# Optimization experiments

Hardware: AMD Instinct MI355X
Metric: run time of the kernel (lower is better)

## Reference

```python
import jax, jax.numpy as jnp
import numpy as np

B, S = 16, 768
DCOG, DENV, NENV = 64, 32, 8
D, N, L, FF, NC = 512, 64, 6, 2048, 1
DIL = (1, 2, 4, 8)
EPS = 1e-5


def _layer_norm(x, g, b):
    m = x.mean(-1, keepdims=True)
    v = ((x - m) ** 2).mean(-1, keepdims=True)
    return (x - m) * jax.lax.rsqrt(v + EPS) * g + b


def _conv1d(x, w, b, d):
    # x: (B, D, S), w: (O, I, K); 'same' padding = (K-1)*d//2 = d for K=3
    y = jax.lax.conv_general_dilated(x, w, (1,), [(d, d)], rhs_dilation=(d,),
                                     dimension_numbers=('NCH', 'OIH', 'NCH'))
    return y + b[None, :, None]


def _combine(c1, c2):
    a1, b1 = c1
    a2, b2 = c2
    return a1 * a2, a2 * b1 + b2


def _forward(x_cog, cw1, cb1, cw2, cb2, env_emb, ew1, eb1, ew2, eb2,
             fw1, fb1, fw2, fb2, pos_enc, conv_w, conv_b, wm_w, wm_b,
             ssm_w, ssm_b, A_log, ffw1, ffb1, ffw2, ffb2,
             g1, be1, g2, be2, pw1, pb1, pw2, pb2, x_env):
    # Dual-channel feature processor (dropout = identity at eval)
    z = x_cog / jnp.maximum(jnp.linalg.norm(x_cog, axis=-1, keepdims=True), 1e-12)
    z = jnp.maximum(z @ cw1 + cb1, 0.0) @ cw2 + cb2
    e = env_emb[x_env].mean(-2)                      # (B,S,NENV,D) -> (B,S,D)
    e = jnp.maximum(e @ ew1 + eb1, 0.0) @ ew2 + eb2
    hf = jnp.concatenate([z, e], -1)
    hf = jnp.maximum(hf @ fw1 + fb1, 0.0) @ fw2 + fb2
    h = hf + pos_enc[:S][None]

    def layer_step(h, p):
        cw, cb, wmw, wmb, sw, sb, alog, w1, b1, w2, b2, g1_, be1_, g2_, be2_ = p
        # Multi-scale dilated conv
        xt = h.transpose(0, 2, 1)                    # (B, D, S)
        outs = [_conv1d(xt, cw[i], cb[i], DIL[i]) for i in range(4)]
        alpha = jax.nn.softmax(xt.mean(-1) @ wmw + wmb, -1)   # (B, 4)
        hm = sum(alpha[:, i, None, None] * outs[i] for i in range(4)).transpose(0, 2, 1)
        h1 = _layer_norm(hm + h, g1_, be1_)
        # Selective state-space (diagonal A), parallel associative scan
        proj = jnp.einsum('bsd,kdn->kbsn', h1, sw) + sb[:, None, None, :]
        delta, Bt, Ct = jax.nn.softplus(proj[0]), proj[1], proj[2]
        a = jnp.exp(alog[None, None, :] * delta)     # (B, S, N)
        bu = Bt * h1[..., :N]
        _, hs = jax.lax.associative_scan(_combine, (a, bu), axis=1)
        y = jnp.sum(Ct * hs, -1, keepdims=True)      # (B, S, 1)
        h2 = _layer_norm(y + h1, g2_, be2_)          # broadcast over D, as in torch
        return jnp.maximum(h2 @ w1 + b1, 0.0) @ w2 + b2 + h2, None

    h, _ = jax.lax.scan(layer_step, h, (conv_w, conv_b, wm_w, wm_b, ssm_w, ssm_b,
                                        A_log, ffw1, ffb1, ffw2, ffb2, g1, be1, g2, be2))
    hg = h.mean(1)                                   # adaptive avg pool over S
    return jnp.maximum(hg @ pw1 + pb1, 0.0) @ pw2 + pb2


def setup_inputs():
    ks = iter(jax.random.split(jax.random.key(0), 48))
    def rn(shape, s=0.02):
        return jax.random.normal(next(ks), shape, jnp.float32) * s
    return {
        'x_cog': rn((B, S, DCOG), 1.0),
        'cw1': rn((DCOG, D)), 'cb1': jnp.zeros(D), 'cw2': rn((D, D)), 'cb2': jnp.zeros(D),
        'env_emb': rn((DENV, D), 1.0),
        'ew1': rn((D, D)), 'eb1': jnp.zeros(D), 'ew2': rn((D, D)), 'eb2': jnp.zeros(D),
        'fw1': rn((2 * D, D)), 'fb1': jnp.zeros(D), 'fw2': rn((D, D)), 'fb2': jnp.zeros(D),
        'pos_enc': rn((1000, D), 1.0),
        'conv_w': rn((L, 4, D, D, 3)), 'conv_b': jnp.zeros((L, 4, D)),
        'wm_w': rn((L, D, 4)), 'wm_b': jnp.zeros((L, 4)),
        'ssm_w': rn((L, 3, D, N)), 'ssm_b': jnp.zeros((L, 3, N)),
        'A_log': -jnp.abs(rn((L, N), 1.0)),
        'ffw1': rn((L, D, FF)), 'ffb1': jnp.zeros((L, FF)),
        'ffw2': rn((L, FF, D)), 'ffb2': jnp.zeros((L, D)),
        'g1': jnp.ones((L, D)), 'be1': jnp.zeros((L, D)),
        'g2': jnp.ones((L, D)), 'be2': jnp.zeros((L, D)),
        'pw1': rn((D, D // 2)), 'pb1': jnp.zeros(D // 2),
        'pw2': rn((D // 2, NC)), 'pb2': jnp.zeros(NC),
        'x_env': jax.random.randint(next(ks), (B, S, NENV), 0, DENV, jnp.int32),
    }


def reference(x_cog, cw1, cb1, cw2, cb2, env_emb, ew1, eb1, ew2, eb2,
              fw1, fb1, fw2, fb2, pos_enc, conv_w, conv_b, wm_w, wm_b,
              ssm_w, ssm_b, A_log, ffw1, ffb1, ffw2, ffb2,
              g1, be1, g2, be2, pw1, pb1, pw2, pb2, x_env):
    return _forward(x_cog, cw1, cb1, cw2, cb2, env_emb, ew1, eb1, ew2, eb2,
                    fw1, fb1, fw2, fb2, pos_enc, conv_w, conv_b, wm_w, wm_b,
                    ssm_w, ssm_b, A_log, ffw1, ffb1, ffw2, ffb2,
                    g1, be1, g2, be2, pw1, pb1, pw2, pb2, x_env)
```

## Files before the change

### kernel.cpp

```cpp
#include <hip/hip_runtime.h>
#include <cstdint>
#include <cstddef>

namespace {

constexpr int B = 16, S = 768, BS = B * S, D = 512, FF = 2048, L = 6;
constexpr float EPS = 1e-5f;

typedef float f32x4 __attribute__((ext_vector_type(4)));
typedef _Float16 f16x8 __attribute__((ext_vector_type(8)));

__device__ __forceinline__ float wave_sum(float v) {
#pragma unroll
  for (int o = 32; o > 0; o >>= 1) v += __shfl_xor(v, o, 64);
  return v;
}

__device__ __forceinline__ short f16b(float x) {
  const _Float16 h = (_Float16)x;
  return __builtin_bit_cast(short, h);
}
__device__ __forceinline__ float h2f(short s) {
  return (float)__builtin_bit_cast(_Float16, s);
}

__device__ __forceinline__ void gload16(const void* g, void* l) {
  __builtin_amdgcn_global_load_lds(
      (const __attribute__((address_space(1))) void*)g,
      (__attribute__((address_space(3))) void*)l, 16, 0, 0);
}


template <bool RELU, bool PACK>
__global__ __launch_bounds__(256, 3) void gemm_h(
    const short* __restrict__ A, int lda, const short* __restrict__ Wt,
    int ldw, int Klen, const float* __restrict__ bias,
    short* __restrict__ ph, int ldp) {
  __shared__ alignas(16) short sAh[8192], sBh[8192];
  const int tid = threadIdx.x;
  const unsigned Nt = gridDim.x;
  const unsigned lin = blockIdx.y * Nt + blockIdx.x;
  const unsigned cpx = (Nt * gridDim.y) >> 3;
  const unsigned swz = (lin & 7) * cpx + (lin >> 3);
  const int bn = (int)(swz % Nt) * 128, bm = (int)(swz / Nt) * 128;
  const int wave = tid >> 6, lane = tid & 63;
  const int wr = (wave >> 1) * 64, wc = (wave & 1) * 64;
  const int lr = lane & 15, sl = lane >> 4;
  const short* Ab = A + (size_t)bm * lda;
  const short* Wb = Wt + (size_t)bn * ldw;
  f32x4 acc[4][4] = {};
  for (int kk = 0; kk < Klen; kk += 64) {
#pragma unroll
    for (int jj = 0; jj < 4; ++jj) {
      const int G = jj * 256 + tid;
      const int srow = G >> 3, sl0 = G & 7;
      const int gsl = sl0 ^ (srow & 7);
      const int dst = G * 8;
      gload16(Ab + (size_t)srow * lda + kk + gsl * 8, &sAh[dst]);
      gload16(Wb + (size_t)srow * ldw + kk + gsl * 8, &sBh[dst]);
    }
    __syncthreads();
#pragma unroll
    for (int ks = 0; ks < 2; ++ks) {
      f16x8 aH[4], bH[4];
#pragma unroll
      for (int m = 0; m < 4; ++m) {
        const int r = wr + m * 16 + lr;
        aH[m] = *(const f16x8*)&sAh[r * 64 + (((ks * 4 + sl) ^ (r & 7)) * 8)];
      }
#pragma unroll
      for (int n = 0; n < 4; ++n) {
        const int r = wc + n * 16 + lr;
        bH[n] = *(const f16x8*)&sBh[r * 64 + (((ks * 4 + sl) ^ (r & 7)) * 8)];
      }
#pragma unroll
      for (int m = 0; m < 4; ++m)
#pragma unroll
        for (int n = 0; n < 4; ++n)
          acc[m][n] = __builtin_amdgcn_mfma_f32_16x16x32_f16(aH[m], bH[n],
                                                             acc[m][n], 0, 0, 0);
    }
    __syncthreads();
  }
  const int r4 = sl * 4;
#pragma unroll
  for (int m = 0; m < 4; ++m) {
#pragma unroll
    for (int r = 0; r < 4; ++r) {
      const int mm = bm + wr + m * 16 + r4 + r;
#pragma unroll
      for (int n = 0; n < 4; ++n) {
        const int col = bn + wc + n * 16 + lr;
        float v = acc[m][n][r] + bias[col];
        if (RELU) v = fmaxf(v, 0.f);
        if (PACK) ph[(size_t)mm * ldp + col] = f16b(v);
      }
    }
  }
}

template <bool RELU, int RESM, bool PACK, bool CSUM, int BK>
__global__ __launch_bounds__(256, 3) void gemm_h64(
    const short* __restrict__ A, int lda, const short* __restrict__ Wt,
    int ldw, int Klen, const float* __restrict__ bias,
    const float* __restrict__ resid, const short* __restrict__ residS,
    int ldr, int rmod, short* __restrict__ ph, int ldp,
    float* __restrict__ part) {
  constexpr int GPR = BK / 8;
  constexpr int AR = 128 * GPR / 256;
  constexpr int BR = 64 * GPR / 256;
  constexpr int KS = BK / 32;
  __shared__ alignas(16) short sAh[128 * BK], sBh[64 * BK];
  __shared__ float csLds[2][64];
  const int tid = threadIdx.x;
  const unsigned Nt = gridDim.x;
  const unsigned lin = blockIdx.y * Nt + blockIdx.x;
  const unsigned cpx = (Nt * gridDim.y) >> 3;
  const unsigned swz = (lin & 7) * cpx + (lin >> 3);
  const int bn = (int)(swz % Nt) * 64, bmt = (int)(swz / Nt);
  const int bm = bmt * 128;
  const int wave = tid >> 6, lane = tid & 63;
  const int wr = (wave >> 1) * 64, wc = (wave & 1) * 32;
  const int lr = lane & 15, sl = lane >> 4;
  const short* Ab = A + (size_t)bm * lda;
  const short* Wb = Wt + (size_t)bn * ldw;
  f32x4 acc[4][2] = {};
  for (int kk = 0; kk < Klen; kk += BK) {
#pragma unroll
    for (int jj = 0; jj < AR; ++jj) {
      const int G = jj * 256 + tid;
      const int srow = G / GPR, sl0 = G % GPR;
      const int gsl = sl0 ^ (srow & (GPR - 1));
      gload16(Ab + (size_t)srow * lda + kk + gsl * 8, &sAh[G * 8]);
    }
#pragma unroll
    for (int jj = 0; jj < BR; ++jj) {
      const int G = jj * 256 + tid;
      const int srow = G / GPR, sl0 = G % GPR;
      const int gsl = sl0 ^ (srow & (GPR - 1));
      gload16(Wb + (size_t)srow * ldw + kk + gsl * 8, &sBh[G * 8]);
    }
    __syncthreads();
#pragma unroll
    for (int ks = 0; ks < KS; ++ks) {
      f16x8 aH[4], bH[2];
#pragma unroll
      for (int m = 0; m < 4; ++m) {
        const int r = wr + m * 16 + lr;
        aH[m] = *(const f16x8*)
            &sAh[r * BK + (((ks * 4 + sl) ^ (r & (GPR - 1))) * 8)];
      }
#pragma unroll
      for (int n = 0; n < 2; ++n) {
        const int r = wc + n * 16 + lr;
        bH[n] = *(const f16x8*)
            &sBh[r * BK + (((ks * 4 + sl) ^ (r & (GPR - 1))) * 8)];
      }
#pragma unroll
      for (int m = 0; m < 4; ++m)
#pragma unroll
        for (int n = 0; n < 2; ++n)
          acc[m][n] = __builtin_amdgcn_mfma_f32_16x16x32_f16(aH[m], bH[n],
                                                             acc[m][n], 0, 0, 0);
    }
    __syncthreads();
  }
  const int r4 = sl * 4;
  float cs[2] = {0.f, 0.f};
#pragma unroll
  for (int m = 0; m < 4; ++m) {
#pragma unroll
    for (int r = 0; r < 4; ++r) {
      const int mm = bm + wr + m * 16 + r4 + r;
#pragma unroll
      for (int n = 0; n < 2; ++n) {
        const int col = bn + wc + n * 16 + lr;
        float v = acc[m][n][r] + bias[col];
        if (RELU) v = fmaxf(v, 0.f);
        if (RESM == 1) {
          const int rr = rmod ? (mm % rmod) : mm;
          v += resid[(size_t)rr * ldr + col];
        }
        if (RESM == 2) v += h2f(residS[(size_t)mm * ldr + col]);
        if (PACK) ph[(size_t)mm * ldp + col] = f16b(v);
        if (CSUM) cs[n] += v;
      }
    }
  }
  if constexpr (CSUM) {
#pragma unroll
    for (int n = 0; n < 2; ++n) {
      cs[n] += __shfl_xor(cs[n], 16, 64);
      cs[n] += __shfl_xor(cs[n], 32, 64);
    }
    if (sl == 0) {
      csLds[wave >> 1][wc + lr] = cs[0];
      csLds[wave >> 1][wc + 16 + lr] = cs[1];
    }
    __syncthreads();
    if (tid < 64)
      part[(size_t)bmt * 512 + bn + tid] = csLds[0][tid] + csLds[1][tid];
  }
}

__global__ __launch_bounds__(256, 3) void conv_zp_k(
    const short* __restrict__ hp, const short* __restrict__ wt8,
    const short* __restrict__ wmix, const float* __restrict__ alpha,
    const short* __restrict__ zpadS, short* __restrict__ P) {
  __shared__ alignas(16) short sAh[16384], sBh[8192];
  const int tid = threadIdx.x;
  const unsigned lin = blockIdx.x;
  const unsigned swz = (lin & 7) * 96 + (lin >> 3);
  const int bn = (int)(swz & 7) * 64;
  const int bmt = (int)(swz >> 3);
  const int b = bmt / 6, s0 = (bmt % 6) * 128, gm0 = bmt * 128;
  const int wave = tid >> 6, lane = tid & 63;
  const int wr = (wave >> 1) * 64, wc = (wave & 1) * 32;
  const int lr = lane & 15, sl = lane >> 4;
  const short* hb = hp + (size_t)b * S * 512;
  f32x4 accF[4][2] = {};
#pragma unroll
  for (int z = 0; z < 4; ++z) {
    const int dd = 1 << z;
    f32x4 acc[4][2] = {};
    for (int kk = 0; kk < 1024; kk += 128) {
      const int tap = kk >> 9;
      const int koff = kk & 511;
      const int off = tap ? dd : -dd;
#pragma unroll
      for (int jj = 0; jj < 8; ++jj) {
        const int G = jj * 256 + tid;
        const int srow = G >> 4, sl0 = G & 15;
        const int gsl = sl0 ^ (srow & 15);
        const int gs = s0 + srow + off;
        const bool inb = ((unsigned)gs < (unsigned)S);
        const short* aBase = hb + (size_t)gs * 512 + koff + gsl * 8;
        gload16(inb ? aBase : zpadS, &sAh[G * 8]);
      }
#pragma unroll
      for (int jj = 0; jj < 4; ++jj) {
        const int G = jj * 256 + tid;
        const int srow = G >> 4, sl0 = G & 15;
        const int gsl = sl0 ^ (srow & 15);
        gload16(wt8 + ((size_t)((z * 2 + tap) * 512 + bn + srow)) * 512 +
                    koff + gsl * 8,
                &sBh[G * 8]);
      }
      __syncthreads();
#pragma unroll
      for (int ks = 0; ks < 4; ++ks) {
        f16x8 aH[4], bH[2];
#pragma unroll
        for (int m = 0; m < 4; ++m) {
          const int r = wr + m * 16 + lr;
          aH[m] = *(const f16x8*)
              &sAh[r * 128 + (((ks * 4 + sl) ^ (r & 15)) * 8)];
        }
#pragma unroll
        for (int n = 0; n < 2; ++n) {
          const int r = wc + n * 16 + lr;
          bH[n] = *(const f16x8*)
              &sBh[r * 128 + (((ks * 4 + sl) ^ (r & 15)) * 8)];
        }
#pragma unroll
        for (int m = 0; m < 4; ++m)
#pragma unroll
          for (int n = 0; n < 2; ++n)
            acc[m][n] = __builtin_amdgcn_mfma_f32_16x16x32_f16(
                aH[m], bH[n], acc[m][n], 0, 0, 0);
      }
      __syncthreads();
    }
    const float al = alpha[b * 4 + z];
#pragma unroll
    for (int m = 0; m < 4; ++m)
#pragma unroll
      for (int n = 0; n < 2; ++n)
#pragma unroll
        for (int r = 0; r < 4; ++r) accF[m][n][r] += al * acc[m][n][r];
  }
  const short* Wm = wmix + (size_t)b * 512 * 512;
  for (int kc = 0; kc < 512; kc += 128) {
#pragma unroll
    for (int jj = 0; jj < 8; ++jj) {
      const int G = jj * 256 + tid;
      const int srow = G >> 4, sl0 = G & 15;
      const int gsl = sl0 ^ (srow & 15);
      gload16(hb + (size_t)(s0 + srow) * 512 + kc + gsl * 8, &sAh[G * 8]);
    }
#pragma unroll
    for (int jj = 0; jj < 4; ++jj) {
      const int G = jj * 256 + tid;
      const int srow = G >> 4, sl0 = G & 15;
      const int gsl = sl0 ^ (srow & 15);
      gload16(Wm + (size_t)(bn + srow) * 512 + kc + gsl * 8, &sBh[G * 8]);
    }
    __syncthreads();
#pragma unroll
    for (int ks = 0; ks < 4; ++ks) {
      f16x8 aH[4], bH[2];
#pragma unroll
      for (int m = 0; m < 4; ++m) {
        const int r = wr + m * 16 + lr;
        aH[m] =
            *(const f16x8*)&sAh[r * 128 + (((ks * 4 + sl) ^ (r & 15)) * 8)];
      }
#pragma unroll
      for (int n = 0; n < 2; ++n) {
        const int r = wc + n * 16 + lr;
        bH[n] =
            *(const f16x8*)&sBh[r * 128 + (((ks * 4 + sl) ^ (r & 15)) * 8)];
      }
#pragma unroll
      for (int m = 0; m < 4; ++m)
#pragma unroll
        for (int n = 0; n < 2; ++n)
          accF[m][n] = __builtin_amdgcn_mfma_f32_16x16x32_f16(
              aH[m], bH[n], accF[m][n], 0, 0, 0);
    }
    __syncthreads();
  }
  const int r4 = sl * 4;
#pragma unroll
  for (int m = 0; m < 4; ++m)
#pragma unroll
    for (int r = 0; r < 4; ++r) {
      const int mm = gm0 + wr + m * 16 + r4 + r;
#pragma unroll
      for (int n = 0; n < 2; ++n)
        P[(size_t)mm * D + bn + wc + n * 16 + lr] = f16b(accF[m][n][r]);
    }
}

__global__ __launch_bounds__(256) void ln3_k(
    const short* __restrict__ P0, const short* __restrict__ hpk,
    const float* __restrict__ cbmix, const float* __restrict__ g1,
    const float* __restrict__ b1, const float* __restrict__ g2,
    const float* __restrict__ b2, short* __restrict__ pout) {
  const int row = blockIdx.x * 4 + (threadIdx.x >> 6);
  const int lane = threadIdx.x & 63;
  const int bb = row / S;
  const size_t base = (size_t)row * D;
  float v[8];
  float s = 0.f;
#pragma unroll
  for (int j = 0; j < 8; ++j) {
    const int c = lane + 64 * j;
    v[j] = h2f(P0[base + c]) + h2f(hpk[base + c]) + cbmix[(size_t)bb * D + c];
    s += v[j];
  }
  s = wave_sum(s);
  const float m1 = s * (1.f / D);
  float q = 0.f;
#pragma unroll
  for (int j = 0; j < 8; ++j) { const float d = v[j] - m1; q += d * d; }
  q = wave_sum(q);
  const float r1 = rsqrtf(q * (1.f / D) + EPS);
  float y[8];
  float s2 = 0.f;
#pragma unroll
  for (int j = 0; j < 8; ++j) {
    const int c = lane + 64 * j;
    y[j] = (v[j] - m1) * r1 * g1[c] + b1[c];
    s2 += y[j];
  }
  s2 = wave_sum(s2);
  const float m2 = s2 * (1.f / D);
  float q2 = 0.f;
#pragma unroll
  for (int j = 0; j < 8; ++j) { const float d = y[j] - m2; q2 += d * d; }
  q2 = wave_sum(q2);
  const float r2 = rsqrtf(q2 * (1.f / D) + EPS);
  short* prow = pout + base;
#pragma unroll
  for (int j = 0; j < 8; ++j) {
    const int c = lane + 64 * j;
    prow[c] = f16b((y[j] - m2) * r2 * g2[c] + b2[c]);
  }
}

__device__ __forceinline__ void pack_tile(const float* __restrict__ W,
                                          short* __restrict__ out, int K,
                                          int N, int n0, int k0) {
  __shared__ short t[64][68];
  const int ln = threadIdx.x & 63, w4 = threadIdx.x >> 6;
#pragma unroll
  for (int it = 0; it < 16; ++it) {
    const int kr = it * 4 + w4;
    t[kr][ln] = f16b(W[(size_t)(k0 + kr) * N + n0 + ln]);
  }
  __syncthreads();
#pragma unroll
  for (int it = 0; it < 16; ++it) {
    const int nr = it * 4 + w4;
    out[(size_t)(n0 + nr) * K + k0 + ln] = t[ln][nr];
  }
}

__global__ __launch_bounds__(256) void pack_wt_k(const float* __restrict__ W,
                                                 short* __restrict__ out,
                                                 int K, int N) {
  pack_tile(W, out, K, N, blockIdx.x * 64, blockIdx.y * 64);
}

__global__ __launch_bounds__(256) void pack_ff_all_k(
    const float* __restrict__ ffw1, const float* __restrict__ ffw2,
    short* __restrict__ outAll) {
  const int bid = blockIdx.x;
  const int l = bid >> 9;
  const int r = bid & 511;
  if (r < 256) {
    pack_tile(ffw1 + (size_t)l * D * FF, outAll + (size_t)l * 2097152, 512,
              2048, (r & 31) * 64, (r >> 5) * 64);
  } else {
    const int r2 = r - 256;
    pack_tile(ffw2 + (size_t)l * FF * D,
              outAll + (size_t)l * 2097152 + 1048576, 2048, 512,
              (r2 & 7) * 64, (r2 >> 3) * 64);
  }
}

__global__ __launch_bounds__(256) void pack_conv8_all_k(
    const float* __restrict__ cw, short* __restrict__ out) {
  const size_t idx = (size_t)blockIdx.x * 256 + threadIdx.x;
  const int c = (int)(idx & 511);
  const int o = (int)((idx >> 9) & 511);
  const int seg = (int)((idx >> 18) & 7);
  const int l = (int)(idx >> 21);
  const int z = seg >> 1, t = (seg & 1) * 2;
  out[idx] = f16b(cw[((size_t)l * 4 * D * D + ((size_t)z * D + o) * D + c) * 3 + t]);
}

__global__ __launch_bounds__(256) void wmix_k(const float* __restrict__ cw,
                                              const float* __restrict__ alpha,
                                              short* __restrict__ wm) {
  __shared__ float sal[64];
  if (threadIdx.x < 64) sal[threadIdx.x] = alpha[threadIdx.x];
  __syncthreads();
  const int idx = blockIdx.x * 256 + threadIdx.x;
  const int c = idx & 511, o = idx >> 9;
  float w[4];
#pragma unroll
  for (int z = 0; z < 4; ++z)
    w[z] = cw[(((size_t)z * D + o) * D + c) * 3 + 1];
#pragma unroll
  for (int b = 0; b < 16; ++b) {
    const float v = sal[b * 4 + 0] * w[0] + sal[b * 4 + 1] * w[1] +
                    sal[b * 4 + 2] * w[2] + sal[b * 4 + 3] * w[3];
    wm[((size_t)b * D + o) * D + c] = f16b(v);
  }
}

__global__ __launch_bounds__(256) void zero_k(float* __restrict__ p) {
  p[threadIdx.x] = 0.f;
  p[threadIdx.x + 256] = 0.f;
}

__global__ __launch_bounds__(64) void alpha_k(const float* __restrict__ part,
                                              const float* __restrict__ wmw,
                                              const float* __restrict__ wmb,
                                              const float* __restrict__ cb,
                                              float* __restrict__ alpha,
                                              float* __restrict__ cbmix) {
  const int b = blockIdx.x, t = threadIdx.x;
  float p0 = 0, p1 = 0, p2 = 0, p3 = 0;
  for (int d = t; d < D; d += 64) {
    float xm = 0;
#pragma unroll
    for (int c = 0; c < 6; ++c) xm += part[((size_t)(b * 6 + c)) * D + d];
    xm *= (1.f / S);
    p0 += xm * wmw[d * 4 + 0];
    p1 += xm * wmw[d * 4 + 1];
    p2 += xm * wmw[d * 4 + 2];
    p3 += xm * wmw[d * 4 + 3];
  }
  p0 = wave_sum(p0); p1 = wave_sum(p1);
  p2 = wave_sum(p2); p3 = wave_sum(p3);
  const float l0 = p0 + wmb[0], l1 = p1 + wmb[1];
  const float l2 = p2 + wmb[2], l3 = p3 + wmb[3];
  const float mx = fmaxf(fmaxf(l0, l1), fmaxf(l2, l3));
  const float e0 = expf(l0 - mx), e1 = expf(l1 - mx);
  const float e2 = expf(l2 - mx), e3 = expf(l3 - mx);
  const float inv = 1.f / (e0 + e1 + e2 + e3);
  const float a0 = e0 * inv, a1 = e1 * inv, a2 = e2 * inv, a3 = e3 * inv;
  if (t == 0) {
    alpha[b * 4 + 0] = a0;
    alpha[b * 4 + 1] = a1;
    alpha[b * 4 + 2] = a2;
    alpha[b * 4 + 3] = a3;
  }
  for (int c = t; c < D; c += 64)
    cbmix[(size_t)b * D + c] =
        a0 * cb[c] + a1 * cb[D + c] + a2 * cb[2 * D + c] + a3 * cb[3 * D + c];
}

__global__ __launch_bounds__(256) void embed_k(const int* __restrict__ xe,
                                               const float* __restrict__ emb,
                                               short* __restrict__ out) {
  const int r = blockIdx.x;
  int idx[8];
#pragma unroll
  for (int j = 0; j < 8; ++j) idx[j] = xe[r * 8 + j];
  short* o = out + (size_t)r * 512;
  for (int d = threadIdx.x; d < D; d += 256) {
    float s = 0.f;
#pragma unroll
    for (int j = 0; j < 8; ++j) s += emb[(size_t)idx[j] * D + d];
    o[d] = f16b(s * 0.125f);
  }
}

__global__ __launch_bounds__(256) void norml2_k(const float* __restrict__ x,
                                                short* __restrict__ out) {
  const int r = blockIdx.x * 4 + (threadIdx.x >> 6);
  const int lane = threadIdx.x & 63;
  const float v = x[(size_t)r * 64 + lane];
  const float s = wave_sum(v * v);
  const float nrm = fmaxf(sqrtf(s), 1e-12f);
  out[(size_t)r * 64 + lane] = f16b(v / nrm);
}

__global__ __launch_bounds__(256) void head_k(
    const float* __restrict__ part, const float* __restrict__ pw1,
    const float* __restrict__ pb1, const float* __restrict__ pw2,
    const float* __restrict__ pb2, float* __restrict__ out) {
  __shared__ float hg[D];
  __shared__ float red[256];
  const int b = blockIdx.x, t = threadIdx.x;
  for (int d = t; d < D; d += 256) {
    float s = 0.f;
#pragma unroll
    for (int c = 0; c < 6; ++c) s += part[((size_t)(b * 6 + c)) * D + d];
    hg[d] = s * (1.f / S);
  }
  __syncthreads();
  float s = pb1[t];
  for (int d = 0; d < D; ++d) s = fmaf(hg[d], pw1[(size_t)d * 256 + t], s);
  s = fmaxf(s, 0.f);
  red[t] = s * pw2[t];
  __syncthreads();
  for (int o = 128; o > 0; o >>= 1) {
    if (t < o) red[t] += red[t + o];
    __syncthreads();
  }
  if (t == 0) out[b] = red[0] + pb2[0];
}

}

extern "C" void kernel_launch(void* const* d_in, const int* in_sizes, int n_in,
                              void* d_out, int out_size, void* d_ws,
                              size_t ws_size, hipStream_t stream) {
  const float* x_cog = (const float*)d_in[0];
  const float* cw1 = (const float*)d_in[1];
  const float* cb1 = (const float*)d_in[2];
  const float* cw2 = (const float*)d_in[3];
  const float* cb2 = (const float*)d_in[4];
  const float* env_emb = (const float*)d_in[5];
  const float* ew1 = (const float*)d_in[6];
  const float* eb1 = (const float*)d_in[7];
  const float* ew2 = (const float*)d_in[8];
  const float* eb2 = (const float*)d_in[9];
  const float* fw1 = (const float*)d_in[10];
  const float* fb1 = (const float*)d_in[11];
  const float* fw2 = (const float*)d_in[12];
  const float* fb2 = (const float*)d_in[13];
  const float* pos_enc = (const float*)d_in[14];
  const float* conv_w = (const float*)d_in[15];
  const float* conv_b = (const float*)d_in[16];
  const float* wm_w = (const float*)d_in[17];
  const float* wm_b = (const float*)d_in[18];
  const float* ffw1 = (const float*)d_in[22];
  const float* ffb1 = (const float*)d_in[23];
  const float* ffw2 = (const float*)d_in[24];
  const float* ffb2 = (const float*)d_in[25];
  const float* g1 = (const float*)d_in[26];
  const float* be1 = (const float*)d_in[27];
  const float* g2 = (const float*)d_in[28];
  const float* be2 = (const float*)d_in[29];
  const float* pw1 = (const float*)d_in[30];
  const float* pb1 = (const float*)d_in[31];
  const float* pw2 = (const float*)d_in[32];
  const float* pb2 = (const float*)d_in[33];
  const int* x_env = (const int*)d_in[34];
  float* out = (float*)d_out;

  float* ws = (float*)d_ws;
  float* PART2 = ws;
  float* ALPHAB = PART2 + 65536;
  float* ZPADF = ALPHAB + 64;
  float* CBMIX = ZPADF + 512;
  short* R = (short*)(CBMIX + 8192);
  short* WFFALL = R;
  short* WC8ALL = R + 12582912;
  short* WMIX = R + 25165824;
  short* convPh = R + 29360128;
  short* HPACK = R + 35651584;
  short* APFF = R + 41943040;
  short* CONC = APFF;
  short* PK1 = R + 67108864;
  short* PK2 = R + 73400320;
  short* WPBF = R + 79691776;

  const dim3 blk(256);
  const dim3 gS(8, 96, 1);
  const dim3 gF(16, 96, 1);

  zero_k<<<1, blk, 0, stream>>>(ZPADF);
  pack_ff_all_k<<<3072, blk, 0, stream>>>(ffw1, ffw2, WFFALL);
  pack_conv8_all_k<<<49152, blk, 0, stream>>>(conv_w, WC8ALL);

  norml2_k<<<BS / 4, blk, 0, stream>>>(x_cog, PK1);
  pack_wt_k<<<dim3(8, 1), blk, 0, stream>>>(cw1, WPBF, 64, 512);
  gemm_h64<true, 0, true, false, 64><<<gS, blk, 0, stream>>>(
      PK1, 64, WPBF, 64, 64, cb1, nullptr, nullptr, 0, 0, PK2, 512, nullptr);
  pack_wt_k<<<dim3(8, 8), blk, 0, stream>>>(cw2, WPBF, 512, 512);
  gemm_h64<false, 0, true, false, 128><<<gS, blk, 0, stream>>>(
      PK2, 512, WPBF, 512, 512, cb2, nullptr, nullptr, 0, 0, CONC, 2048,
      nullptr);
  embed_k<<<BS, blk, 0, stream>>>(x_env, env_emb, PK1);
  pack_wt_k<<<dim3(8, 8), blk, 0, stream>>>(ew1, WPBF, 512, 512);
  gemm_h64<true, 0, true, false, 128><<<gS, blk, 0, stream>>>(
      PK1, 512, WPBF, 512, 512, eb1, nullptr, nullptr, 0, 0, PK2, 512,
      nullptr);
  pack_wt_k<<<dim3(8, 8), blk, 0, stream>>>(ew2, WPBF, 512, 512);
  gemm_h64<false, 0, true, false, 128><<<gS, blk, 0, stream>>>(
      PK2, 512, WPBF, 512, 512, eb2, nullptr, nullptr, 0, 0, CONC + 512, 2048,
      nullptr);
  pack_wt_k<<<dim3(8, 16), blk, 0, stream>>>(fw1, WPBF, 1024, 512);
  gemm_h64<true, 0, true, false, 128><<<gS, blk, 0, stream>>>(
      CONC, 2048, WPBF, 1024, 1024, fb1, nullptr, nullptr, 0, 0, PK1, 512,
      nullptr);
  pack_wt_k<<<dim3(8, 8), blk, 0, stream>>>(fw2, WPBF, 512, 512);
  gemm_h64<false, 1, true, true, 128><<<gS, blk, 0, stream>>>(
      PK1, 512, WPBF, 512, 512, fb2, pos_enc, nullptr, 512, S, HPACK, 512,
      PART2);

  for (int l = 0; l < L; ++l) {
    const float* cwl = conv_w + (size_t)l * 4 * D * D * 3;
    alpha_k<<<B, dim3(64), 0, stream>>>(PART2, wm_w + (size_t)l * D * 4,
                                        wm_b + l * 4,
                                        conv_b + (size_t)l * 4 * D, ALPHAB,
                                        CBMIX);
    wmix_k<<<1024, blk, 0, stream>>>(cwl, ALPHAB, WMIX);
    conv_zp_k<<<768, blk, 0, stream>>>(HPACK, WC8ALL + (size_t)l * 2097152,
                                       WMIX, ALPHAB, (const short*)ZPADF,
                                       convPh);
    ln3_k<<<BS / 4, blk, 0, stream>>>(convPh, HPACK, CBMIX, g1 + l * D,
                                      be1 + l * D, g2 + l * D, be2 + l * D,
                                      HPACK);
    gemm_h<true, true><<<gF, blk, 0, stream>>>(
        HPACK, 512, WFFALL + (size_t)l * 2097152, 512, 512,
        ffb1 + (size_t)l * FF, APFF, 2048);
    gemm_h64<false, 2, true, true, 128><<<gS, blk, 0, stream>>>(
        APFF, 2048, WFFALL + (size_t)l * 2097152 + 1048576, 2048, 2048,
        ffb2 + (size_t)l * D, nullptr, HPACK, 512, 0, HPACK, 512, PART2);
  }

  head_k<<<B, blk, 0, stream>>>(PART2, pw1, pb1, pw2, pb2, out);
}
```

Before: 1.245 ms.

## Split dilated conv GEMM across dilation pairs with 128x128 tiles and two partial outputs

Result: faster. 1.143 ms (-8.2%).

```diff
diff --git a/kernel.cpp b/kernel.cpp
--- a/kernel.cpp
+++ b/kernel.cpp
@@ -207,65 +207,63 @@
     const short* __restrict__ hp, const short* __restrict__ wt8,
     const short* __restrict__ wmix, const float* __restrict__ alpha,
     const short* __restrict__ zpadS, short* __restrict__ P) {
-  __shared__ alignas(16) short sAh[16384], sBh[8192];
+  __shared__ alignas(16) short sAh[8192], sBh[8192];
   const int tid = threadIdx.x;
   const unsigned lin = blockIdx.x;
   const unsigned swz = (lin & 7) * 96 + (lin >> 3);
-  const int bn = (int)(swz & 7) * 64;
-  const int bmt = (int)(swz >> 3);
+  const int zp = (int)(swz / 384);
+  const unsigned rem = swz % 384;
+  const int bn = (int)(rem & 3) * 128;
+  const int bmt = (int)(rem >> 2);
   const int b = bmt / 6, s0 = (bmt % 6) * 128, gm0 = bmt * 128;
   const int wave = tid >> 6, lane = tid & 63;
-  const int wr = (wave >> 1) * 64, wc = (wave & 1) * 32;
+  const int wr = (wave >> 1) * 64, wc = (wave & 1) * 64;
   const int lr = lane & 15, sl = lane >> 4;
   const short* hb = hp + (size_t)b * S * 512;
-  f32x4 accF[4][2] = {};
-#pragma unroll
-  for (int z = 0; z < 4; ++z) {
+  f32x4 accF[4][4] = {};
+#pragma unroll
+  for (int zi = 0; zi < 2; ++zi) {
+    const int z = zp * 2 + zi;
     const int dd = 1 << z;
-    f32x4 acc[4][2] = {};
-    for (int kk = 0; kk < 1024; kk += 128) {
+    f32x4 acc[4][4] = {};
+    for (int kk = 0; kk < 1024; kk += 64) {
       const int tap = kk >> 9;
       const int koff = kk & 511;
       const int off = tap ? dd : -dd;
 #pragma unroll
-      for (int jj = 0; jj < 8; ++jj) {
+      for (int jj = 0; jj < 4; ++jj) {
         const int G = jj * 256 + tid;
-        const int srow = G >> 4, sl0 = G & 15;
-        const int gsl = sl0 ^ (srow & 15);
+        const int srow = G >> 3, sl0 = G & 7;
+        const int gsl = sl0 ^ (srow & 7);
+        const int dst = G * 8;
         const int gs = s0 + srow + off;
         const bool inb = ((unsigned)gs < (unsigned)S);
         const short* aBase = hb + (size_t)gs * 512 + koff + gsl * 8;
-        gload16(inb ? aBase : zpadS, &sAh[G * 8]);
-      }
-#pragma unroll
-      for (int jj = 0; jj < 4; ++jj) {
-        const int G = jj * 256 + tid;
-        const int srow = G >> 4, sl0 = G & 15;
-        const int gsl = sl0 ^ (srow & 15);
+        gload16(inb ? aBase : zpadS, &sAh[dst]);
         gload16(wt8 + ((size_t)((z * 2 + tap) * 512 + bn + srow)) * 512 +
                     koff + gsl * 8,
-                &sBh[G * 8]);
+                &sBh[dst]);
       }
       __syncthreads();
 #pragma unroll
-      for (int ks = 0; ks < 4; ++ks) {
-        f16x8 aH[4], bH[2];
+      for (int ks = 0; ks < 2; ++ks) {
+        f16x8 aH[4], bH[4];
 #pragma unroll
         for (int m = 0; m < 4; ++m) {
           const int r = wr + m * 16 + lr;
-          aH[m] = *(const f16x8*)
-              &sAh[r * 128 + (((ks * 4 + sl) ^ (r & 15)) * 8)];
+          aH[m] =
+              *(const f16x8*)&sAh[r * 64 + (((ks * 4 + sl) ^ (r & 7)) * 8)];
         }
 #pragma unroll
-        for (int n = 0; n < 2; ++n) {
+        for (int n = 0; n < 4; ++n) {
           const int r = wc + n * 16 + lr;
-          bH[n] = *(const f16x8*)
-              &sBh[r * 128 + (((ks * 4 + sl) ^ (r & 15)) * 8)];
+          bH[n] =
+              *(const f16x8*)&sBh[r * 64 + (((ks * 4 + sl) ^ (r & 7)) * 8)];
         }
 #pragma unroll
         for (int m = 0; m < 4; ++m)
 #pragma unroll
-          for (int n = 0; n < 2; ++n)
+          for (int n = 0; n < 4; ++n)
             acc[m][n] = __builtin_amdgcn_mfma_f32_16x16x32_f16(
                 aH[m], bH[n], acc[m][n], 0, 0, 0);
       }
@@ -275,51 +273,46 @@
 #pragma unroll
     for (int m = 0; m < 4; ++m)
 #pragma unroll
-      for (int n = 0; n < 2; ++n)
+      for (int n = 0; n < 4; ++n)
 #pragma unroll
         for (int r = 0; r < 4; ++r) accF[m][n][r] += al * acc[m][n][r];
   }
   const short* Wm = wmix + (size_t)b * 512 * 512;
-  for (int kc = 0; kc < 512; kc += 128) {
-#pragma unroll
-    for (int jj = 0; jj < 8; ++jj) {
-      const int G = jj * 256 + tid;
-      const int srow = G >> 4, sl0 = G & 15;
-      const int gsl = sl0 ^ (srow & 15);
-      gload16(hb + (size_t)(s0 + srow) * 512 + kc + gsl * 8, &sAh[G * 8]);
-    }
+  for (int kc = 0; kc < 256; kc += 64) {
+    const int koff = zp * 256 + kc;
 #pragma unroll
     for (int jj = 0; jj < 4; ++jj) {
       const int G = jj * 256 + tid;
-      const int srow = G >> 4, sl0 = G & 15;
-      const int gsl = sl0 ^ (srow & 15);
-      gload16(Wm + (size_t)(bn + srow) * 512 + kc + gsl * 8, &sBh[G * 8]);
-    }
-    __syncthreads();
-#pragma unroll
-    for (int ks = 0; ks < 4; ++ks) {
-      f16x8 aH[4], bH[2];
+      const int srow = G >> 3, sl0 = G & 7;
+      const int gsl = sl0 ^ (srow & 7);
+      const int dst = G * 8;
+      gload16(hb + (size_t)(s0 + srow) * 512 + koff + gsl * 8, &sAh[dst]);
+      gload16(Wm + (size_t)(bn + srow) * 512 + koff + gsl * 8, &sBh[dst]);
+    }
+    __syncthreads();
+#pragma unroll
+    for (int ks = 0; ks < 2; ++ks) {
+      f16x8 aH[4], bH[4];
 #pragma unroll
       for (int m = 0; m < 4; ++m) {
         const int r = wr + m * 16 + lr;
-        aH[m] =
-            *(const f16x8*)&sAh[r * 128 + (((ks * 4 + sl) ^ (r & 15)) * 8)];
-      }
-#pragma unroll
-      for (int n = 0; n < 2; ++n) {
+        aH[m] = *(const f16x8*)&sAh[r * 64 + (((ks * 4 + sl) ^ (r & 7)) * 8)];
+      }
+#pragma unroll
+      for (int n = 0; n < 4; ++n) {
         const int r = wc + n * 16 + lr;
-        bH[n] =
-            *(const f16x8*)&sBh[r * 128 + (((ks * 4 + sl) ^ (r & 15)) * 8)];
+        bH[n] = *(const f16x8*)&sBh[r * 64 + (((ks * 4 + sl) ^ (r & 7)) * 8)];
       }
 #pragma unroll
       for (int m = 0; m < 4; ++m)
 #pragma unroll
-        for (int n = 0; n < 2; ++n)
+        for (int n = 0; n < 4; ++n)
           accF[m][n] = __builtin_amdgcn_mfma_f32_16x16x32_f16(
               aH[m], bH[n], accF[m][n], 0, 0, 0);
     }
     __syncthreads();
   }
+  short* Pz = P + (size_t)zp * ((size_t)BS * D);
   const int r4 = sl * 4;
 #pragma unroll
   for (int m = 0; m < 4; ++m)
@@ -327,16 +320,17 @@
     for (int r = 0; r < 4; ++r) {
       const int mm = gm0 + wr + m * 16 + r4 + r;
 #pragma unroll
-      for (int n = 0; n < 2; ++n)
-        P[(size_t)mm * D + bn + wc + n * 16 + lr] = f16b(accF[m][n][r]);
+      for (int n = 0; n < 4; ++n)
+        Pz[(size_t)mm * D + bn + wc + n * 16 + lr] = f16b(accF[m][n][r]);
     }
 }
 
 __global__ __launch_bounds__(256) void ln3_k(
-    const short* __restrict__ P0, const short* __restrict__ hpk,
-    const float* __restrict__ cbmix, const float* __restrict__ g1,
-    const float* __restrict__ b1, const float* __restrict__ g2,
-    const float* __restrict__ b2, short* __restrict__ pout) {
+    const short* __restrict__ P0, const short* __restrict__ P1,
+    const short* __restrict__ hpk, const float* __restrict__ cbmix,
+    const float* __restrict__ g1, const float* __restrict__ b1,
+    const float* __restrict__ g2, const float* __restrict__ b2,
+    short* __restrict__ pout) {
   const int row = blockIdx.x * 4 + (threadIdx.x >> 6);
   const int lane = threadIdx.x & 63;
   const int bb = row / S;
@@ -346,7 +340,8 @@
 #pragma unroll
   for (int j = 0; j < 8; ++j) {
     const int c = lane + 64 * j;
-    v[j] = h2f(P0[base + c]) + h2f(hpk[base + c]) + cbmix[(size_t)bb * D + c];
+    v[j] = h2f(P0[base + c]) + h2f(P1[base + c]) + h2f(hpk[base + c]) +
+           cbmix[(size_t)bb * D + c];
     s += v[j];
   }
   s = wave_sum(s);
@@ -428,7 +423,8 @@
   const int seg = (int)((idx >> 18) & 7);
   const int l = (int)(idx >> 21);
   const int z = seg >> 1, t = (seg & 1) * 2;
-  out[idx] = f16b(cw[((size_t)l * 4 * D * D + ((size_t)z * D + o) * D + c) * 3 + t]);
+  out[idx] =
+      f16b(cw[((size_t)l * 4 * D * D + ((size_t)z * D + o) * D + c) * 3 + t]);
 }
 
 __global__ __launch_bounds__(256) void wmix_k(const float* __restrict__ cw,
@@ -595,12 +591,12 @@
   short* WC8ALL = R + 12582912;
   short* WMIX = R + 25165824;
   short* convPh = R + 29360128;
-  short* HPACK = R + 35651584;
-  short* APFF = R + 41943040;
+  short* HPACK = R + 41943040;
+  short* APFF = R + 48234496;
   short* CONC = APFF;
-  short* PK1 = R + 67108864;
-  short* PK2 = R + 73400320;
-  short* WPBF = R + 79691776;
+  short* PK1 = R + 73400320;
+  short* PK2 = R + 79691776;
+  short* WPBF = R + 85983232;
 
   const dim3 blk(256);
   const dim3 gS(8, 96, 1);
@@ -646,9 +642,9 @@
     conv_zp_k<<<768, blk, 0, stream>>>(HPACK, WC8ALL + (size_t)l * 2097152,
                                        WMIX, ALPHAB, (const short*)ZPADF,
                                        convPh);
-    ln3_k<<<BS / 4, blk, 0, stream>>>(convPh, HPACK, CBMIX, g1 + l * D,
-                                      be1 + l * D, g2 + l * D, be2 + l * D,
-                                      HPACK);
+    ln3_k<<<BS / 4, blk, 0, stream>>>(convPh, convPh + (size_t)BS * D, HPACK,
+                                      CBMIX, g1 + l * D, be1 + l * D,
+                                      g2 + l * D, be2 + l * D, HPACK);
     gemm_h<true, true><<<gF, blk, 0, stream>>>(
         HPACK, 512, WFFALL + (size_t)l * 2097152, 512, 512,
         ffb1 + (size_t)l * FF, APFF, 2048);
```
